# Kernel tuning notes

Hardware: AMD Instinct MI355X
Metric: run time of the kernel (lower is better)

Reference implementation:

```python
import jax, jax.numpy as jnp
import numpy as np

N = 10000        # nodes
E = 320000       # edges
IN_DIM = 512
H_DIM = 256
HEADS = 8
HEAD_D = H_DIM // HEADS
OUT_DIM = 40
NEG_SLOPE = 0.2  # standard GAT LeakyReLU slope


def setup_inputs() -> dict:
    key = jax.random.key(0)
    ks = jax.random.split(key, 13)
    g = lambda k, shape, scale: (jax.random.normal(k, shape, jnp.float32) * scale)
    x = jax.random.normal(ks[0], (N, IN_DIM), jnp.float32)
    edge_index = jax.random.randint(ks[1], (2, E), 0, N, jnp.int32)
    return {
        "x": x,
        "edge_index": edge_index,
        "W_in": g(ks[2], (IN_DIM, H_DIM), 1.0 / np.sqrt(IN_DIM)),
        "b_in": jnp.zeros((H_DIM,), jnp.float32),
        "W1": g(ks[3], (H_DIM, HEADS, HEAD_D), 1.0 / np.sqrt(H_DIM)),
        "a1_src": g(ks[4], (HEADS, HEAD_D), 1.0 / np.sqrt(HEAD_D)),
        "a1_dst": g(ks[5], (HEADS, HEAD_D), 1.0 / np.sqrt(HEAD_D)),
        "W2": g(ks[6], (H_DIM, HEADS, HEAD_D), 1.0 / np.sqrt(H_DIM)),
        "a2_src": g(ks[7], (HEADS, HEAD_D), 1.0 / np.sqrt(HEAD_D)),
        "a2_dst": g(ks[8], (HEADS, HEAD_D), 1.0 / np.sqrt(HEAD_D)),
        "W_out": g(ks[9], (H_DIM, OUT_DIM), 1.0 / np.sqrt(H_DIM)),
        "b_out": jnp.zeros((OUT_DIM,), jnp.float32),
    }


def _gat_layer(h, src, dst, W, a_src, a_dst):
    # h: [N, H_DIM] -> per-head projections [N, HEADS, HEAD_D]
    Wh = jnp.einsum("nf,fhd->nhd", h, W)
    # additive attention logits, split into src/dst halves of a^T [Wh_i || Wh_j]
    alpha_s = jnp.einsum("nhd,hd->nh", Wh, a_src)   # [N, H]
    alpha_d = jnp.einsum("nhd,hd->nh", Wh, a_dst)   # [N, H]
    e = jax.nn.leaky_relu(alpha_s[src] + alpha_d[dst], NEG_SLOPE)  # [E, H]
    # segment softmax over incoming edges of each destination node
    m = jax.ops.segment_max(e, dst, num_segments=N)                # [N, H]
    m = jnp.where(jnp.isfinite(m), m, 0.0)
    p = jnp.exp(e - m[dst])                                        # [E, H]
    denom = jax.ops.segment_sum(p, dst, num_segments=N)            # [N, H]
    attn = p / jnp.maximum(denom[dst], 1e-9)                       # [E, H]
    msg = attn[:, :, None] * Wh[src]                               # [E, H, D]
    out = jax.ops.segment_sum(msg, dst, num_segments=N)            # [N, H, D]
    return out.reshape(N, HEADS * HEAD_D)                          # head concat


def reference(x, edge_index, W_in, b_in, W1, a1_src, a1_dst, W2, a2_src, a2_dst, W_out, b_out):
    src, dst = edge_index[0], edge_index[1]
    h = x @ W_in + b_in                                  # input linear
    h = jax.nn.relu(_gat_layer(h, src, dst, W1, a1_src, a1_dst))
    h = jax.nn.relu(_gat_layer(h, src, dst, W2, a2_src, a2_dst))
    return h @ W_out + b_out                             # output head
```

## Files before the change

### kernel.cpp

```cpp
#include <hip/hip_runtime.h>
#include <hip/hip_bf16.h>

#define NN 10000
#define NE 320000
#define IND 512
#define HD 256
#define NH 8
#define OD 40
#define NEG 0.2f
#define MAXD 96

typedef __attribute__((ext_vector_type(8))) short bf16x8;
typedef __attribute__((ext_vector_type(4))) float f32x4;

__device__ __forceinline__ float bf2f(unsigned short u){
    return __uint_as_float(((unsigned)u) << 16);
}
__device__ __forceinline__ unsigned short f2bf(float v){
    __hip_bfloat16 h = __float2bfloat16(v);
    return *(unsigned short*)&h;
}

__device__ __forceinline__ int wave_flag(const unsigned short* __restrict__ w){
    float av = fabsf(bf2f(w[threadIdx.x & 63]));
    return (__popcll(__ballot(!(av < 0.5f))) < 4) ? 1 : 0;
}

__global__ __launch_bounds__(256)
void k_prep(const void* __restrict__ x_p, const void* __restrict__ Win_p,
            const void* __restrict__ W1_p, const void* __restrict__ W2_p,
            const void* __restrict__ Wo_p,
            const void* __restrict__ bin_p, const void* __restrict__ a1s_p,
            const void* __restrict__ a1d_p, const void* __restrict__ a2s_p,
            const void* __restrict__ a2d_p, const void* __restrict__ bo_p,
            unsigned short* __restrict__ xb, unsigned short* __restrict__ WinT,
            unsigned short* __restrict__ W1T, unsigned short* __restrict__ W2T,
            unsigned short* __restrict__ WoT,
            float* __restrict__ binf, float* __restrict__ a1sf, float* __restrict__ a1df,
            float* __restrict__ a2sf, float* __restrict__ a2df, float* __restrict__ bof,
            int* __restrict__ cnt){
    __shared__ float tile[32][33];
    int b = blockIdx.x, t = threadIdx.x;
    int flag = wave_flag((const unsigned short*)Win_p);

    if (b < 2500){
        if (!flag){
            int i = b*256 + t;
            const float4* f = (const float4*)x_p;
            float4 a = f[i*2], c = f[i*2+1];
            ushort4 o0, o1;
            o0.x=f2bf(a.x); o0.y=f2bf(a.y); o0.z=f2bf(a.z); o0.w=f2bf(a.w);
            o1.x=f2bf(c.x); o1.y=f2bf(c.y); o1.z=f2bf(c.z); o1.w=f2bf(c.w);
            ((ushort4*)xb)[i*2] = o0; ((ushort4*)xb)[i*2+1] = o1;
        }
        return;
    }
    b -= 2500;
    if (b == 272){
        int f = flag;
        #define CV(p,i) (f ? bf2f(((const unsigned short*)(p))[i]) : ((const float*)(p))[i])
        if (t < 256){
            binf[t] = CV(bin_p,t);
            a1sf[t] = CV(a1s_p,t); a1df[t] = CV(a1d_p,t);
            a2sf[t] = CV(a2s_p,t); a2df[t] = CV(a2d_p,t);
        }
        if (t < OD) bof[t] = CV(bo_p,t);
        #undef CV
        return;
    }
    if (b > 272){
        int i = (b - 273)*256 + t;
        if (i < NN) cnt[i] = 0;
        return;
    }
    const void* Bp; unsigned short* BTp; int K, N, NP, bx, by;
    if (b < 128){ Bp=Win_p; BTp=WinT; K=IND; N=HD; NP=HD; bx=b&15; by=b>>4; }
    else if (b < 192){ int c=b-128; Bp=W1_p; BTp=W1T; K=HD; N=HD; NP=HD; bx=c&7; by=c>>3; }
    else if (b < 256){ int c=b-192; Bp=W2_p; BTp=W2T; K=HD; N=HD; NP=HD; bx=c&7; by=c>>3; }
    else { int c=b-256; Bp=Wo_p; BTp=WoT; K=HD; N=OD; NP=64; bx=c&7; by=c>>3; }
    int k0 = bx*32, n0 = by*32, tx = t & 31, ty = t >> 5;
    #pragma unroll
    for (int i = 0; i < 4; i++){
        int k = k0 + ty + i*8, n = n0 + tx;
        float v = 0.f;
        if (n < N){
            v = flag ? bf2f(((const unsigned short*)Bp)[(size_t)k*N + n])
                     : ((const float*)Bp)[(size_t)k*N + n];
        }
        tile[ty + i*8][tx] = v;
    }
    __syncthreads();
    #pragma unroll
    for (int i = 0; i < 4; i++){
        int n = n0 + ty + i*8, k = k0 + tx;
        if (n < NP) BTp[(size_t)n*K + k] = f2bf(tile[tx][ty + i*8]);
    }
}

template<int BN, int ALPHA, int FLAGOUT, int FILL>
__global__ __launch_bounds__(256)
void k_mfma(const unsigned short* __restrict__ A, const unsigned short* __restrict__ Aalt,
            const unsigned short* __restrict__ flagsrc,
            const unsigned short* __restrict__ BT, const float* __restrict__ bias,
            void* __restrict__ C,
            const float* __restrict__ asrc, const float* __restrict__ adst,
            float* __restrict__ als, float* __restrict__ ald,
            int M, int N, int K,
            int gemmBX, const int* __restrict__ srcE, const int* __restrict__ dstE,
            int* __restrict__ cnt, int* __restrict__ col2d){
    constexpr int BM = 64, BK = 64, LDR = BK + 8;
    constexpr int MI = (BN == 128) ? 2 : 1;
    constexpr int NJ = 4;
    __shared__ unsigned short As[BM * LDR];
    __shared__ unsigned short Bs[BN * LDR];
    int t = threadIdx.x, lane = t & 63, wid = t >> 6;

    if (FILL){
        if ((int)blockIdx.x >= gemmBX){
            int e = ((blockIdx.x - gemmBX)*gridDim.y + blockIdx.y)*256 + t;
            if (e < NE){
                int d = dstE[e];
                int p = atomicAdd(&cnt[d], 1);
                if (p < MAXD) col2d[(size_t)d*MAXD + p] = srcE[e];
            }
            return;
        }
    }

    int roff, coff;
    if (BN == 128){ roff = (wid >> 1) * 32; coff = (wid & 1) * 64; }
    else          { roff = wid * 16;        coff = 0; }
    int rowBase = blockIdx.x * BM;
    int colBase = blockIdx.y * BN;

    int flag = 1;
    if (FLAGOUT || Aalt != nullptr) flag = wave_flag(flagsrc);
    const unsigned short* Ause = (Aalt != nullptr && flag) ? Aalt : A;

    f32x4 acc[MI][NJ] = {};

    int arow = rowBase + (t >> 2); if (arow >= M) arow = M - 1;
    const unsigned short* Ag = Ause + (size_t)arow * K + (t & 3) * 16;
    unsigned short* Asw = &As[(t >> 2) * LDR + (t & 3) * 16];
    const unsigned short* Bg;
    unsigned short* Bsw;
    if (BN == 128){ Bg = BT + (size_t)(colBase + (t >> 1)) * K + (t & 1)*32; Bsw = &Bs[(t >> 1) * LDR + (t & 1)*32]; }
    else          { Bg = BT + (size_t)(colBase + (t >> 2)) * K + (t & 3)*16; Bsw = &Bs[(t >> 2) * LDR + (t & 3)*16]; }

    for (int k0 = 0; k0 < K; k0 += BK){
        *(bf16x8*)(Asw)     = *(const bf16x8*)(Ag + k0);
        *(bf16x8*)(Asw + 8) = *(const bf16x8*)(Ag + k0 + 8);
        if (BN == 128){
            #pragma unroll
            for (int c = 0; c < 4; c++)
                *(bf16x8*)(Bsw + c*8) = *(const bf16x8*)(Bg + k0 + c*8);
        } else {
            *(bf16x8*)(Bsw)     = *(const bf16x8*)(Bg + k0);
            *(bf16x8*)(Bsw + 8) = *(const bf16x8*)(Bg + k0 + 8);
        }
        __syncthreads();
        #pragma unroll
        for (int ks = 0; ks < 2; ks++){
            bf16x8 a[MI], b[NJ];
            #pragma unroll
            for (int mi = 0; mi < MI; mi++)
                a[mi] = *(const bf16x8*)&As[(roff + mi*16 + (lane & 15)) * LDR + ks*32 + (lane >> 4)*8];
            #pragma unroll
            for (int nj = 0; nj < NJ; nj++)
                b[nj] = *(const bf16x8*)&Bs[(coff + nj*16 + (lane & 15)) * LDR + ks*32 + (lane >> 4)*8];
            #pragma unroll
            for (int mi = 0; mi < MI; mi++)
                #pragma unroll
                for (int nj = 0; nj < NJ; nj++)
                    acc[mi][nj] = __builtin_amdgcn_mfma_f32_16x16x32_bf16(a[mi], b[nj], acc[mi][nj], 0, 0, 0);
        }
        __syncthreads();
    }

    if (ALPHA){
        int hbase = (colBase + coff) >> 5;
        float as_v[NJ], ad_v[NJ];
        #pragma unroll
        for (int nj = 0; nj < NJ; nj++){
            int c = colBase + coff + nj*16 + (lane & 15);
            as_v[nj] = asrc[c]; ad_v[nj] = adst[c];
        }
        #pragma unroll
        for (int mi = 0; mi < MI; mi++){
            #pragma unroll
            for (int r = 0; r < 4; r++){
                int row = rowBase + roff + mi*16 + (lane >> 4)*4 + r;
                #pragma unroll
                for (int hg = 0; hg < 2; hg++){
                    float ps = acc[mi][2*hg][r]*as_v[2*hg] + acc[mi][2*hg+1][r]*as_v[2*hg+1];
                    float pd = acc[mi][2*hg][r]*ad_v[2*hg] + acc[mi][2*hg+1][r]*ad_v[2*hg+1];
                    ps += __shfl_xor(ps, 1); pd += __shfl_xor(pd, 1);
                    ps += __shfl_xor(ps, 2); pd += __shfl_xor(pd, 2);
                    ps += __shfl_xor(ps, 4); pd += __shfl_xor(pd, 4);
                    ps += __shfl_xor(ps, 8); pd += __shfl_xor(pd, 8);
                    if ((lane & 15) == 0 && row < M){
                        als[row * NH + hbase + hg] = ps;
                        ald[row * NH + hbase + hg] = pd;
                    }
                }
            }
        }
    }

    #pragma unroll
    for (int mi = 0; mi < MI; mi++){
        #pragma unroll
        for (int nj = 0; nj < NJ; nj++){
            int col = colBase + coff + nj*16 + (lane & 15);
            #pragma unroll
            for (int r = 0; r < 4; r++){
                int row = rowBase + roff + mi*16 + (lane >> 4)*4 + r;
                if (row < M && col < N){
                    float v = acc[mi][nj][r] + (bias ? bias[col] : 0.f);
                    if (FLAGOUT){
                        if (flag) ((unsigned short*)C)[(size_t)row * N + col] = f2bf(v);
                        else      ((float*)C)[(size_t)row * N + col] = v;
                    } else {
                        ((unsigned short*)C)[(size_t)row * N + col] = f2bf(v);
                    }
                }
            }
        }
    }
}

__global__ __launch_bounds__(256)
void k_agg(const int* __restrict__ cnt, const int* __restrict__ col2d,
           const unsigned short* __restrict__ Wh, const float* __restrict__ als,
           const float* __restrict__ ald, unsigned short* __restrict__ out){
    __shared__ float pshm[4][64*NH];
    __shared__ int scol[4][64];
    int t = threadIdx.x, lane = t & 63, wid = t >> 6;
    float* psh = pshm[wid];
    int* sc = scol[wid];
    int hL = lane >> 3;

    int node = blockIdx.x*4 + wid;
    if (node >= NN) return;

    int deg = cnt[node]; if (deg > MAXD) deg = MAXD;
    const int* cols = col2d + (size_t)node * MAXD;
    float ad[NH];
    {
        float4 v0 = *(const float4*)&ald[node * NH];
        float4 v1 = *(const float4*)&ald[node * NH + 4];
        ad[0]=v0.x; ad[1]=v0.y; ad[2]=v0.z; ad[3]=v0.w;
        ad[4]=v1.x; ad[5]=v1.y; ad[6]=v1.z; ad[7]=v1.w;
    }
    float den[NH];
    #pragma unroll
    for (int h = 0; h < NH; h++) den[h] = 0.f;
    float4 acc = make_float4(0.f, 0.f, 0.f, 0.f);

    for (int cb = 0; cb < deg; cb += 64){
        int ne_ = min(64, deg - cb);
        float dp[NH];
        if (lane < ne_){
            int s = cols[cb + lane];
            sc[lane] = s;
            float4 v0 = *(const float4*)&als[(size_t)s * NH];
            float4 v1 = *(const float4*)&als[(size_t)s * NH + 4];
            float av[NH] = {v0.x,v0.y,v0.z,v0.w,v1.x,v1.y,v1.z,v1.w};
            #pragma unroll
            for (int h = 0; h < NH; h++){
                float v = av[h] + ad[h];
                v = v > 0.f ? v : NEG * v;
                float p = __expf(fminf(v, 80.f));
                psh[lane*NH + h] = p;
                dp[h] = p;
            }
        } else {
            #pragma unroll
            for (int h = 0; h < NH; h++) dp[h] = 0.f;
        }
        #pragma unroll
        for (int off = 1; off < 64; off <<= 1){
            #pragma unroll
            for (int h = 0; h < NH; h++) dp[h] += __shfl_xor(dp[h], off);
        }
        #pragma unroll
        for (int h = 0; h < NH; h++) den[h] += dp[h];
        asm volatile("s_waitcnt lgkmcnt(0)" ::: "memory");
        int j = 0;
        for (; j + 8 <= ne_; j += 8){
            int s[8]; ushort4 w[8]; float p[8];
            #pragma unroll
            for (int q = 0; q < 8; q++) s[q] = sc[j+q];
            #pragma unroll
            for (int q = 0; q < 8; q++) w[q] = *(const ushort4*)&Wh[(size_t)s[q] * HD + (lane << 2)];
            #pragma unroll
            for (int q = 0; q < 8; q++) p[q] = psh[(j+q)*NH + hL];
            #pragma unroll
            for (int q = 0; q < 8; q++){
                acc.x += p[q]*bf2f(w[q].x); acc.y += p[q]*bf2f(w[q].y);
                acc.z += p[q]*bf2f(w[q].z); acc.w += p[q]*bf2f(w[q].w);
            }
        }
        for (; j < ne_; j++){
            int s = sc[j];
            float p = psh[j*NH + hL];
            ushort4 wv = *(const ushort4*)&Wh[(size_t)s * HD + (lane << 2)];
            acc.x += p * bf2f(wv.x); acc.y += p * bf2f(wv.y);
            acc.z += p * bf2f(wv.z); acc.w += p * bf2f(wv.w);
        }
        asm volatile("s_waitcnt lgkmcnt(0)" ::: "memory");
    }
    float inv = 1.f / fmaxf(den[hL], 1e-9f);
    ushort4 o;
    o.x = f2bf(fmaxf(acc.x * inv, 0.f));
    o.y = f2bf(fmaxf(acc.y * inv, 0.f));
    o.z = f2bf(fmaxf(acc.z * inv, 0.f));
    o.w = f2bf(fmaxf(acc.w * inv, 0.f));
    *(ushort4*)&out[(size_t)node * HD + (lane << 2)] = o;
}

extern "C" void kernel_launch(void* const* d_in, const int* in_sizes, int n_in,
                              void* d_out, int out_size, void* d_ws, size_t ws_size,
                              hipStream_t stream){
    const void* x_p   = d_in[0];
    const int*  eidx  = (const int*)d_in[1];
    const void* Win_p = d_in[2];
    const void* bin_p = d_in[3];
    const void* W1_p  = d_in[4];
    const void* a1s_p = d_in[5];
    const void* a1d_p = d_in[6];
    const void* W2_p  = d_in[7];
    const void* a2s_p = d_in[8];
    const void* a2d_p = d_in[9];
    const void* Wo_p  = d_in[10];
    const void* bo_p  = d_in[11];

    char* base = (char*)d_ws;
    size_t off = 0;
    auto alloc = [&](size_t bytes){ void* p = base + off; off = (off + bytes + 255) & ~255ULL; return p; };

    unsigned short* xb   = (unsigned short*)alloc((size_t)NN * IND * 2);
    unsigned short* WinT = (unsigned short*)alloc((size_t)HD * IND * 2);
    unsigned short* W1T  = (unsigned short*)alloc((size_t)HD * HD * 2);
    unsigned short* W2T  = (unsigned short*)alloc((size_t)HD * HD * 2);
    unsigned short* WoT  = (unsigned short*)alloc((size_t)64 * HD * 2);
    float* binf = (float*)alloc(HD * 4);
    float* a1sf = (float*)alloc(HD * 4);
    float* a1df = (float*)alloc(HD * 4);
    float* a2sf = (float*)alloc(HD * 4);
    float* a2df = (float*)alloc(HD * 4);
    float* bof  = (float*)alloc(64 * 4);
    unsigned short* h1b = (unsigned short*)alloc((size_t)NN * HD * 2);
    unsigned short* Whb = (unsigned short*)alloc((size_t)NN * HD * 2);
    unsigned short* h2b = (unsigned short*)alloc((size_t)NN * HD * 2);
    float* als  = (float*)alloc((size_t)NN * NH * 4);
    float* ald  = (float*)alloc((size_t)NN * NH * 4);
    int* col2d  = (int*)alloc((size_t)NN * MAXD * 4);
    int* cnt    = (int*)alloc(NN * 4);
    unsigned short* h3b = h1b;

    const int* src = eidx;
    const int* dst = eidx + NE;
    const unsigned short* fsrc = (const unsigned short*)Win_p;

    auto cdiv = [](int a, int b){ return (a + b - 1) / b; };
    int gm = cdiv(NN, 64);

    k_prep<<<2813,256,0,stream>>>(x_p, Win_p, W1_p, W2_p, Wo_p,
                                  bin_p, a1s_p, a1d_p, a2s_p, a2d_p, bo_p,
                                  xb, WinT, W1T, W2T, WoT,
                                  binf, a1sf, a1df, a2sf, a2df, bof, cnt);

    k_mfma<128,0,0,1><<<dim3(gm + 625, 2),256,0,stream>>>(
        xb, (const unsigned short*)x_p, fsrc, WinT, binf, h1b,
        nullptr, nullptr, nullptr, nullptr, NN, HD, IND,
        gm, src, dst, cnt, col2d);

    k_mfma<128,1,0,0><<<dim3(gm,2),256,0,stream>>>(
        h1b, nullptr, fsrc, W1T, nullptr, Whb,
        a1sf, a1df, als, ald, NN, HD, HD, 0, nullptr, nullptr, nullptr, nullptr);
    k_agg<<<cdiv(NN,4),256,0,stream>>>(cnt, col2d, Whb, als, ald, h2b);

    k_mfma<128,1,0,0><<<dim3(gm,2),256,0,stream>>>(
        h2b, nullptr, fsrc, W2T, nullptr, Whb,
        a2sf, a2df, als, ald, NN, HD, HD, 0, nullptr, nullptr, nullptr, nullptr);
    k_agg<<<cdiv(NN,4),256,0,stream>>>(cnt, col2d, Whb, als, ald, h3b);

    k_mfma<64,0,1,0><<<dim3(gm,1),256,0,stream>>>(
        h3b, nullptr, fsrc, WoT, bof, d_out,
        nullptr, nullptr, nullptr, nullptr, NN, OD, HD, 0, nullptr, nullptr, nullptr, nullptr);
}
```

Before: 208.3 us.

## Split wave into two half-waves gathering 16-byte rows and fold denominator into accumulation

The aggregation kernel now has each half of the wave handle alternate edges, with every lane loading 8 bf16 values (16 bytes) per neighbor row instead of 4. The halves are combined with one cross-half shuffle at the end. The softmax denominator is no longer computed by a 6-step butterfly reduction over all 8 heads per chunk. Each lane instead accumulates the weights of its own head alongside the message sum. This cuts shuffle work and doubles the number of edges in flight per instruction, at the cost of more accumulator registers and an extra final reduction.

```diff
diff --git a/kernel.cpp b/kernel.cpp
--- a/kernel.cpp
+++ b/kernel.cpp
@@ -11,6 +11,7 @@
 #define MAXD 96
 
 typedef __attribute__((ext_vector_type(8))) short bf16x8;
+typedef __attribute__((ext_vector_type(8))) unsigned short u16x8;
 typedef __attribute__((ext_vector_type(4))) float f32x4;
 
 __device__ __forceinline__ float bf2f(unsigned short u){
@@ -238,7 +239,10 @@
     int t = threadIdx.x, lane = t & 63, wid = t >> 6;
     float* psh = pshm[wid];
     int* sc = scol[wid];
-    int hL = lane >> 3;
+    int half = lane >> 5;
+    int l32 = lane & 31;
+    int ch0 = l32 * 8;
+    int hL = l32 >> 2;
 
     int node = blockIdx.x*4 + wid;
     if (node >= NN) return;
@@ -252,14 +256,11 @@
         ad[0]=v0.x; ad[1]=v0.y; ad[2]=v0.z; ad[3]=v0.w;
         ad[4]=v1.x; ad[5]=v1.y; ad[6]=v1.z; ad[7]=v1.w;
     }
-    float den[NH];
-    #pragma unroll
-    for (int h = 0; h < NH; h++) den[h] = 0.f;
-    float4 acc = make_float4(0.f, 0.f, 0.f, 0.f);
+    float accv[8] = {0.f,0.f,0.f,0.f,0.f,0.f,0.f,0.f};
+    float dsum = 0.f;
 
     for (int cb = 0; cb < deg; cb += 64){
         int ne_ = min(64, deg - cb);
-        float dp[NH];
         if (lane < ne_){
             int s = cols[cb + lane];
             sc[lane] = s;
@@ -270,53 +271,49 @@
             for (int h = 0; h < NH; h++){
                 float v = av[h] + ad[h];
                 v = v > 0.f ? v : NEG * v;
-                float p = __expf(fminf(v, 80.f));
-                psh[lane*NH + h] = p;
-                dp[h] = p;
-            }
-        } else {
-            #pragma unroll
-            for (int h = 0; h < NH; h++) dp[h] = 0.f;
-        }
-        #pragma unroll
-        for (int off = 1; off < 64; off <<= 1){
-            #pragma unroll
-            for (int h = 0; h < NH; h++) dp[h] += __shfl_xor(dp[h], off);
-        }
-        #pragma unroll
-        for (int h = 0; h < NH; h++) den[h] += dp[h];
+                psh[lane*NH + h] = __expf(fminf(v, 80.f));
+            }
+        }
         asm volatile("s_waitcnt lgkmcnt(0)" ::: "memory");
         int j = 0;
-        for (; j + 8 <= ne_; j += 8){
-            int s[8]; ushort4 w[8]; float p[8];
-            #pragma unroll
-            for (int q = 0; q < 8; q++) s[q] = sc[j+q];
-            #pragma unroll
-            for (int q = 0; q < 8; q++) w[q] = *(const ushort4*)&Wh[(size_t)s[q] * HD + (lane << 2)];
-            #pragma unroll
-            for (int q = 0; q < 8; q++) p[q] = psh[(j+q)*NH + hL];
+        for (; j + 16 <= ne_; j += 16){
+            int s[8]; u16x8 w[8]; float p[8];
+            #pragma unroll
+            for (int q = 0; q < 8; q++) s[q] = sc[j + 2*q + half];
+            #pragma unroll
+            for (int q = 0; q < 8; q++) w[q] = *(const u16x8*)&Wh[(size_t)s[q] * HD + ch0];
+            #pragma unroll
+            for (int q = 0; q < 8; q++) p[q] = psh[(j + 2*q + half)*NH + hL];
             #pragma unroll
             for (int q = 0; q < 8; q++){
-                acc.x += p[q]*bf2f(w[q].x); acc.y += p[q]*bf2f(w[q].y);
-                acc.z += p[q]*bf2f(w[q].z); acc.w += p[q]*bf2f(w[q].w);
-            }
-        }
-        for (; j < ne_; j++){
-            int s = sc[j];
-            float p = psh[j*NH + hL];
-            ushort4 wv = *(const ushort4*)&Wh[(size_t)s * HD + (lane << 2)];
-            acc.x += p * bf2f(wv.x); acc.y += p * bf2f(wv.y);
-            acc.z += p * bf2f(wv.z); acc.w += p * bf2f(wv.w);
+                dsum += p[q];
+                #pragma unroll
+                for (int k = 0; k < 8; k++) accv[k] += p[q] * bf2f(w[q][k]);
+            }
+        }
+        for (; j < ne_; j += 2){
+            int r = j + half;
+            if (r < ne_){
+                int s = sc[r];
+                u16x8 w = *(const u16x8*)&Wh[(size_t)s * HD + ch0];
+                float p = psh[r*NH + hL];
+                dsum += p;
+                #pragma unroll
+                for (int k = 0; k < 8; k++) accv[k] += p * bf2f(w[k]);
+            }
         }
         asm volatile("s_waitcnt lgkmcnt(0)" ::: "memory");
     }
-    float inv = 1.f / fmaxf(den[hL], 1e-9f);
-    ushort4 o;
-    o.x = f2bf(fmaxf(acc.x * inv, 0.f));
-    o.y = f2bf(fmaxf(acc.y * inv, 0.f));
-    o.z = f2bf(fmaxf(acc.z * inv, 0.f));
-    o.w = f2bf(fmaxf(acc.w * inv, 0.f));
-    *(ushort4*)&out[(size_t)node * HD + (lane << 2)] = o;
+    dsum += __shfl_xor(dsum, 32);
+    #pragma unroll
+    for (int k = 0; k < 8; k++) accv[k] += __shfl_xor(accv[k], 32);
+    if (half == 0){
+        float inv = 1.f / fmaxf(dsum, 1e-9f);
+        u16x8 o;
+        #pragma unroll
+        for (int k = 0; k < 8; k++) o[k] = f2bf(fmaxf(accv[k] * inv, 0.f));
+        *(u16x8*)&out[(size_t)node * HD + ch0] = o;
+    }
 }
 
 extern "C" void kernel_launch(void* const* d_in, const int* in_sizes, int n_in,
```

Measured after the change: 199.8 us. 1.04x faster.
